# Kernel optimization log

Measured on AMD Instinct MI355X. Metric: run time of the kernel, lower is better.

Reference implementation:

```python
import jax, jax.numpy as jnp
import numpy as np

VOCAB, H, L, NUM_LABELS = 32000, 512, 5, 20


def setup_inputs() -> dict:
    key = jax.random.key(0)
    ks = jax.random.split(key, 8)
    B, T = 64, 512
    inputs = jax.random.randint(ks[0], (B, T), 0, VOCAB, dtype=jnp.int32)
    s = 1.0 / np.sqrt(H)
    emb = jax.random.normal(ks[1], (VOCAB, H), jnp.float32) * 0.02
    emb = emb.at[0].set(0.0)  # padding_idx=0
    W_ih = jax.random.uniform(ks[2], (L, 4 * H, H), jnp.float32, -s, s)
    W_hh = jax.random.uniform(ks[3], (L, 4 * H, H), jnp.float32, -s, s)
    b_ih = jax.random.uniform(ks[4], (L, 4 * H), jnp.float32, -s, s)
    b_hh = jax.random.uniform(ks[5], (L, 4 * H), jnp.float32, -s, s)
    W_cls = jax.random.uniform(ks[6], (NUM_LABELS, H), jnp.float32, -s, s)
    b_cls = jax.random.uniform(ks[7], (NUM_LABELS,), jnp.float32, -s, s)
    return {"inputs": inputs, "emb": emb, "W_ih": W_ih, "W_hh": W_hh,
            "b_ih": b_ih, "b_hh": b_hh, "W_cls": W_cls, "b_cls": b_cls}


def _lstm_layer(x, Wih, Whh, bih, bhh):
    # x: [B, T, H] -> [B, T, H]. PyTorch gate order: i, f, g, o.
    B, T, Hd = x.shape
    xg = jnp.einsum('bth,gh->btg', x, Wih) + bih + bhh  # precompute input gates [B,T,4H]

    def step(carry, xt):
        h, c = carry
        g = xt + h @ Whh.T
        i, f, gg, o = jnp.split(g, 4, axis=-1)
        c = jax.nn.sigmoid(f) * c + jax.nn.sigmoid(i) * jnp.tanh(gg)
        h = jax.nn.sigmoid(o) * jnp.tanh(c)
        return (h, c), h

    h0 = jnp.zeros((B, Hd), x.dtype)
    (_, _), ys = jax.lax.scan(step, (h0, h0), jnp.swapaxes(xg, 0, 1))
    return jnp.swapaxes(ys, 0, 1)


def reference(inputs, emb, W_ih, W_hh, b_ih, b_hh, W_cls, b_cls):
    # Dropout between layers is inactive in eval mode; omitted (deterministic baseline).
    x = emb[inputs]  # [B, T, H]
    for l in range(W_ih.shape[0]):
        x = _lstm_layer(x, W_ih[l], W_hh[l], b_ih[l], b_hh[l])
    feature = x[:, -1]  # last timestep hidden of top layer
    return feature @ W_cls.T + b_cls
```

## Files before the change

kernel.cpp:

```cpp
#include <hip/hip_runtime.h>
#include <cmath>

#define BB 64
#define TT 512
#define HH 512
#define GG 2048
#define TCH 64
#define LDT 132

template<bool GATHER>
__global__ __launch_bounds__(256) void xg_gemm(
    const float* __restrict__ Xsrc, const int* __restrict__ tok,
    const float* __restrict__ Wih, const float* __restrict__ bih,
    const float* __restrict__ bhh, float* __restrict__ XG, int t0)
{
  __shared__ float As[32 * LDT];
  __shared__ float Bs[32 * LDT];
  const int tid = threadIdx.x;
  const int tc = tid & 15, tr = tid >> 4;
  const int m0 = blockIdx.x * 128;
  const int g0 = blockIdx.y * 128;

  float acc[8][8];
#pragma unroll
  for (int i = 0; i < 8; ++i)
#pragma unroll
    for (int j = 0; j < 8; ++j) acc[i][j] = 0.f;

  float4 ra[4], rb[4];
#pragma unroll
  for (int i = 0; i < 4; ++i) {
    const int f = tid + i * 256;
    ra[i] = *(const float4*)&Wih[(size_t)(g0 + (f >> 3)) * HH + ((f & 7) << 2)];
  }
#pragma unroll
  for (int i = 0; i < 4; ++i) {
    const int f = tid + i * 256;
    if (GATHER) {
      const int m = m0 + (f >> 3);
      const int tok_i = tok[(m & 63) * TT + t0 + (m >> 6)];
      rb[i] = *(const float4*)&Xsrc[(size_t)tok_i * HH + ((f & 7) << 2)];
    } else {
      rb[i] = *(const float4*)&Xsrc[((size_t)(t0 + (m0 >> 6) + (f >> 9)) * HH
                                     + ((f >> 4) & 31)) * BB + ((f & 15) << 2)];
    }
  }

  for (int kt = 0; kt < 16; ++kt) {
#pragma unroll
    for (int i = 0; i < 4; ++i) {
      const int f = tid + i * 256;
      const int row = f >> 3, c4 = f & 7, s = c4 & 3;
      const int col = (((row >> 2) ^ s) << 2) + (row & 3);
      As[(c4 * 4 + 0) * LDT + col] = ra[i].x;
      As[(c4 * 4 + 1) * LDT + col] = ra[i].y;
      As[(c4 * 4 + 2) * LDT + col] = ra[i].z;
      As[(c4 * 4 + 3) * LDT + col] = ra[i].w;
    }
#pragma unroll
    for (int i = 0; i < 4; ++i) {
      const int f = tid + i * 256;
      if (GATHER) {
        const int row = f >> 3, c4 = f & 7, s = c4 & 3;
        const int col = (((row >> 2) ^ s) << 2) + (row & 3);
        Bs[(c4 * 4 + 0) * LDT + col] = rb[i].x;
        Bs[(c4 * 4 + 1) * LDT + col] = rb[i].y;
        Bs[(c4 * 4 + 2) * LDT + col] = rb[i].z;
        Bs[(c4 * 4 + 3) * LDT + col] = rb[i].w;
      } else {
        const int kk = (f >> 4) & 31, s = (kk >> 2) & 3;
        const int mq = (((f >> 9) << 4) + (f & 15)) ^ s;
        *(float4*)&Bs[kk * LDT + (mq << 2)] = rb[i];
      }
    }
    __syncthreads();
    if (kt < 15) {
      const int k0 = (kt + 1) * 32;
#pragma unroll
      for (int i = 0; i < 4; ++i) {
        const int f = tid + i * 256;
        ra[i] = *(const float4*)&Wih[(size_t)(g0 + (f >> 3)) * HH + k0 + ((f & 7) << 2)];
      }
#pragma unroll
      for (int i = 0; i < 4; ++i) {
        const int f = tid + i * 256;
        if (GATHER) {
          const int m = m0 + (f >> 3);
          const int tok_i = tok[(m & 63) * TT + t0 + (m >> 6)];
          rb[i] = *(const float4*)&Xsrc[(size_t)tok_i * HH + k0 + ((f & 7) << 2)];
        } else {
          rb[i] = *(const float4*)&Xsrc[((size_t)(t0 + (m0 >> 6) + (f >> 9)) * HH
                                         + k0 + ((f >> 4) & 31)) * BB + ((f & 15) << 2)];
        }
      }
    }
#pragma unroll
    for (int k = 0; k < 32; ++k) {
      const int s = (k >> 2) & 3;
      const float4 a0 = *(const float4*)&As[k * LDT + ((tr ^ s) << 2)];
      const float4 a1 = *(const float4*)&As[k * LDT + ((16 + (tr ^ s)) << 2)];
      const float4 b0 = *(const float4*)&Bs[k * LDT + ((tc ^ s) << 2)];
      const float4 b1 = *(const float4*)&Bs[k * LDT + ((16 + (tc ^ s)) << 2)];
      const float av[8] = {a0.x, a0.y, a0.z, a0.w, a1.x, a1.y, a1.z, a1.w};
      const float bv[8] = {b0.x, b0.y, b0.z, b0.w, b1.x, b1.y, b1.z, b1.w};
#pragma unroll
      for (int i2 = 0; i2 < 8; ++i2)
#pragma unroll
        for (int j2 = 0; j2 < 8; ++j2)
          acc[i2][j2] = fmaf(av[i2], bv[j2], acc[i2][j2]);
    }
    __syncthreads();
  }

#pragma unroll
  for (int ah = 0; ah < 2; ++ah)
#pragma unroll
    for (int i = 0; i < 4; ++i) {
      const int gc = g0 + ah * 64 + tr * 4 + i;
      const float bias = bih[gc] + bhh[gc];
#pragma unroll
      for (int bh = 0; bh < 2; ++bh) {
        const int tl_ = (m0 >> 6) + bh;
        float4 v;
        v.x = acc[ah * 4 + i][bh * 4 + 0] + bias;
        v.y = acc[ah * 4 + i][bh * 4 + 1] + bias;
        v.z = acc[ah * 4 + i][bh * 4 + 2] + bias;
        v.w = acc[ah * 4 + i][bh * 4 + 3] + bias;
        *(float4*)&XG[((size_t)tl_ * GG + gc) * BB + (tc << 2)] = v;
      }
    }
}

__global__ __launch_bounds__(256, 1) void lstm_chunk(
    const float* __restrict__ XG, const float* __restrict__ Whh,
    float* __restrict__ h0, float* __restrict__ h1,
    float* __restrict__ c, float* __restrict__ Y,
    unsigned* __restrict__ bar, int t0, int l)
{
  const int tid = threadIdx.x;
  const int grp = blockIdx.x & 7;
  const int mid = blockIdx.x >> 3;
  const int rp = tid >> 3;
  const int ks = tid & 7;
  const int lr0 = 2 * rp, lr1 = 2 * rp + 1;
  const int gc0 = ((lr0 >> 4) << 9) + mid * 16 + (lr0 & 15);
  const int gc1 = ((lr1 >> 4) << 9) + mid * 16 + (lr1 & 15);

  __shared__ float4 hs4[8 * 136];
  __shared__ float gs[512];

  float4 w0[16], w1[16];
#pragma unroll
  for (int cc = 0; cc < 16; ++cc) {
    w0[cc] = *(const float4*)&Whh[(size_t)gc0 * HH + ks * 64 + cc * 4];
    w1[cc] = *(const float4*)&Whh[(size_t)gc1 * HH + ks * 64 + cc * 4];
  }

  const int hc_l = tid >> 3;
  const int bb_l = tid & 7;
  const int hc_own = mid * 16 + hc_l;
  const int Bg_own = 8 * grp + bb_l;
  float creg = 0.f;
  if (t0 > 0 && tid < 128) creg = c[(size_t)hc_own * BB + Bg_own];

  for (int tl = 0; tl < TCH; ++tl) {
    const int t = t0 + tl;
    const int first = (t == 0) ? 1 : 0;
    const float* h_in = (t & 1) ? h1 : h0;
    float* h_out = (t & 1) ? h0 : h1;

    if (!first) {
#pragma unroll
      for (int i = 0; i < 4; ++i) {
        const int f4 = tid + i * 256;
        const int b = f4 >> 7, c4 = f4 & 127;
        const float* src = &h_in[(size_t)(8 * grp + b) * HH + (c4 << 2)];
        float4 v;
        v.x = __hip_atomic_load(src + 0, __ATOMIC_RELAXED, __HIP_MEMORY_SCOPE_AGENT);
        v.y = __hip_atomic_load(src + 1, __ATOMIC_RELAXED, __HIP_MEMORY_SCOPE_AGENT);
        v.z = __hip_atomic_load(src + 2, __ATOMIC_RELAXED, __HIP_MEMORY_SCOPE_AGENT);
        v.w = __hip_atomic_load(src + 3, __ATOMIC_RELAXED, __HIP_MEMORY_SCOPE_AGENT);
        hs4[b * 136 + c4 + (c4 >> 4)] = v;
      }
      __syncthreads();

      float p0[8], p1[8];
#pragma unroll
      for (int b = 0; b < 8; ++b) { p0[b] = 0.f; p1[b] = 0.f; }
#pragma unroll
      for (int cc = 0; cc < 16; ++cc) {
#pragma unroll
        for (int b = 0; b < 8; ++b) {
          const float4 hv = hs4[b * 136 + 17 * ks + cc];
          p0[b] += hv.x * w0[cc].x + hv.y * w0[cc].y + hv.z * w0[cc].z + hv.w * w0[cc].w;
          p1[b] += hv.x * w1[cc].x + hv.y * w1[cc].y + hv.z * w1[cc].z + hv.w * w1[cc].w;
        }
      }
#pragma unroll
      for (int b = 0; b < 8; ++b) {
        float v0 = p0[b], v1 = p1[b];
        v0 += __shfl_xor(v0, 1, 64); v0 += __shfl_xor(v0, 2, 64); v0 += __shfl_xor(v0, 4, 64);
        v1 += __shfl_xor(v1, 1, 64); v1 += __shfl_xor(v1, 2, 64); v1 += __shfl_xor(v1, 4, 64);
        p0[b] = v0; p1[b] = v1;
      }
      if (ks == 0) {
#pragma unroll
        for (int b = 0; b < 8; ++b) {
          gs[lr0 * 8 + b] = p0[b];
          gs[lr1 * 8 + b] = p1[b];
        }
      }
    }
    __syncthreads();

    if (tid < 128) {
      float gv[4];
#pragma unroll
      for (int q = 0; q < 4; ++q) {
        const int gc = (q << 9) + hc_own;
        float x = XG[((size_t)tl * GG + gc) * BB + Bg_own];
        if (!first) x += gs[(q * 16 + hc_l) * 8 + bb_l];
        gv[q] = x;
      }
      const float cold = first ? 0.f : creg;
      const float si = 1.f / (1.f + expf(-gv[0]));
      const float sf = 1.f / (1.f + expf(-gv[1]));
      const float so = 1.f / (1.f + expf(-gv[3]));
      const float cn = sf * cold + si * tanhf(gv[2]);
      const float hn = so * tanhf(cn);
      creg = cn;
      __hip_atomic_store(&h_out[(size_t)Bg_own * HH + hc_own], hn,
                         __ATOMIC_RELAXED, __HIP_MEMORY_SCOPE_AGENT);
      Y[((size_t)t * HH + hc_own) * BB + Bg_own] = hn;
    }

    asm volatile("s_waitcnt vmcnt(0)" ::: "memory");
    __syncthreads();
    if (tid == 0) {
      __hip_atomic_fetch_add(&bar[grp * 32], 1u, __ATOMIC_RELAXED, __HIP_MEMORY_SCOPE_AGENT);
      const unsigned tgt = 32u * (unsigned)(l * 512 + t + 1);
      while (__hip_atomic_load(&bar[grp * 32], __ATOMIC_RELAXED, __HIP_MEMORY_SCOPE_AGENT) < tgt)
        __builtin_amdgcn_s_sleep(2);
    }
    __syncthreads();
  }

  if (tid < 128) c[(size_t)hc_own * BB + Bg_own] = creg;
}

__global__ __launch_bounds__(64) void cls_kernel(
    const float* __restrict__ Y, const float* __restrict__ Wcls,
    const float* __restrict__ bcls, float* __restrict__ out)
{
  __shared__ float feat[512];
  const int b = blockIdx.x, tid = threadIdx.x;
  for (int k = tid; k < HH; k += 64)
    feat[k] = Y[((size_t)(TT - 1) * HH + k) * BB + b];
  __syncthreads();
  if (tid < 20) {
    float acc = bcls[tid];
    for (int k = 0; k < HH; ++k) acc = fmaf(feat[k], Wcls[tid * HH + k], acc);
    out[b * 20 + tid] = acc;
  }
}

extern "C" void kernel_launch(void* const* d_in, const int* in_sizes, int n_in,
                              void* d_out, int out_size, void* d_ws, size_t ws_size,
                              hipStream_t stream) {
  (void)in_sizes; (void)n_in; (void)out_size; (void)ws_size;
  const int*   tok  = (const int*)d_in[0];
  const float* emb  = (const float*)d_in[1];
  const float* Wih  = (const float*)d_in[2];
  const float* Whh  = (const float*)d_in[3];
  const float* bih  = (const float*)d_in[4];
  const float* bhh  = (const float*)d_in[5];
  const float* Wcls = (const float*)d_in[6];
  const float* bcls = (const float*)d_in[7];
  float* out = (float*)d_out;

  float* Y  = (float*)d_ws;
  float* XG = Y + (size_t)TT * HH * BB;
  float* h0 = XG + (size_t)TCH * GG * BB;
  float* h1 = h0 + (size_t)BB * HH;
  float* c  = h1 + (size_t)BB * HH;
  unsigned* bar = (unsigned*)(c + (size_t)HH * BB);

  hipMemsetAsync(bar, 0, 8 * 32 * sizeof(unsigned), stream);

  for (int l = 0; l < 5; ++l) {
    const float* wih_l = Wih + (size_t)l * GG * HH;
    const float* whh_l = Whh + (size_t)l * GG * HH;
    const float* bih_l = bih + (size_t)l * GG;
    const float* bhh_l = bhh + (size_t)l * GG;
    for (int t0 = 0; t0 < TT; t0 += TCH) {
      if (l == 0)
        xg_gemm<true><<<dim3(32, 16), 256, 0, stream>>>(emb, tok, wih_l, bih_l, bhh_l, XG, t0);
      else
        xg_gemm<false><<<dim3(32, 16), 256, 0, stream>>>(Y, nullptr, wih_l, bih_l, bhh_l, XG, t0);
      lstm_chunk<<<256, 256, 0, stream>>>(XG, whh_l, h0, h1, c, Y, bar, t0, l);
    }
  }
  cls_kernel<<<64, 64, 0, stream>>>(Y, Wcls, bcls, out);
}
```

Baseline: 33.61 ms.

## Replace atomic counter barrier with per-block flags and remap recurrent matvec

Replaces the per-group atomic fetch_add counter barrier with per-block step flags that each block writes and 32 lanes poll in parallel, so arrival no longer serializes on a single contended atomic. The recurrent matvec is remapped: each thread now holds four gate rows over a 32-wide K slice and reduces across 16 lanes, and the hidden-state load uses vectorized dwordx4 loads with cache-bypass bits instead of scalar atomic loads. The XG input gate values are prefetched before the matvec so their latency overlaps with the h load. The risk is higher register pressure from the 4x8 weight tile, extra shuffle reduction steps, and the correctness of the inline-asm coherence bits.

```diff
diff --git a/kernel.cpp b/kernel.cpp
--- a/kernel.cpp
+++ b/kernel.cpp
@@ -135,26 +135,24 @@
     const float* __restrict__ XG, const float* __restrict__ Whh,
     float* __restrict__ h0, float* __restrict__ h1,
     float* __restrict__ c, float* __restrict__ Y,
-    unsigned* __restrict__ bar, int t0, int l)
+    unsigned* __restrict__ flag, int t0, int l)
 {
   const int tid = threadIdx.x;
   const int grp = blockIdx.x & 7;
   const int mid = blockIdx.x >> 3;
-  const int rp = tid >> 3;
-  const int ks = tid & 7;
-  const int lr0 = 2 * rp, lr1 = 2 * rp + 1;
-  const int gc0 = ((lr0 >> 4) << 9) + mid * 16 + (lr0 & 15);
-  const int gc1 = ((lr1 >> 4) << 9) + mid * 16 + (lr1 & 15);
-
-  __shared__ float4 hs4[8 * 136];
+  const int rp = tid >> 4;
+  const int ks = tid & 15;
+
+  __shared__ float4 hs4[8 * 144];
   __shared__ float gs[512];
 
-  float4 w0[16], w1[16];
-#pragma unroll
-  for (int cc = 0; cc < 16; ++cc) {
-    w0[cc] = *(const float4*)&Whh[(size_t)gc0 * HH + ks * 64 + cc * 4];
-    w1[cc] = *(const float4*)&Whh[(size_t)gc1 * HH + ks * 64 + cc * 4];
-  }
+  float4 w[4][8];
+#pragma unroll
+  for (int j = 0; j < 4; ++j)
+#pragma unroll
+    for (int cc = 0; cc < 8; ++cc)
+      w[j][cc] = *(const float4*)&Whh[(size_t)((j << 9) + mid * 16 + rp) * HH
+                                      + ks * 32 + cc * 4];
 
   const int hc_l = tid >> 3;
   const int bb_l = tid & 7;
@@ -169,46 +167,68 @@
     const float* h_in = (t & 1) ? h1 : h0;
     float* h_out = (t & 1) ? h0 : h1;
 
+    float xgv[4];
+    if (tid < 128) {
+#pragma unroll
+      for (int q = 0; q < 4; ++q)
+        xgv[q] = XG[((size_t)tl * GG + (q << 9) + hc_own) * BB + Bg_own];
+    }
+
+    float p[4][8];
+#pragma unroll
+    for (int j = 0; j < 4; ++j)
+#pragma unroll
+      for (int b = 0; b < 8; ++b) p[j][b] = 0.f;
+
     if (!first) {
+      float4 hv4[4];
 #pragma unroll
       for (int i = 0; i < 4; ++i) {
-        const int f4 = tid + i * 256;
-        const int b = f4 >> 7, c4 = f4 & 127;
+        const int f = tid + i * 256;
+        const int b = f >> 7, c4 = f & 127;
         const float* src = &h_in[(size_t)(8 * grp + b) * HH + (c4 << 2)];
-        float4 v;
-        v.x = __hip_atomic_load(src + 0, __ATOMIC_RELAXED, __HIP_MEMORY_SCOPE_AGENT);
-        v.y = __hip_atomic_load(src + 1, __ATOMIC_RELAXED, __HIP_MEMORY_SCOPE_AGENT);
-        v.z = __hip_atomic_load(src + 2, __ATOMIC_RELAXED, __HIP_MEMORY_SCOPE_AGENT);
-        v.w = __hip_atomic_load(src + 3, __ATOMIC_RELAXED, __HIP_MEMORY_SCOPE_AGENT);
-        hs4[b * 136 + c4 + (c4 >> 4)] = v;
+        asm volatile("global_load_dwordx4 %0, %1, off sc0 sc1"
+                     : "=v"(hv4[i]) : "v"(src));
+      }
+      asm volatile("s_waitcnt vmcnt(0)" ::: "memory");
+      __builtin_amdgcn_sched_barrier(0);
+#pragma unroll
+      for (int i = 0; i < 4; ++i) {
+        const int f = tid + i * 256;
+        const int b = f >> 7, c4 = f & 127;
+        hs4[b * 144 + (c4 >> 3) * 9 + (c4 & 7)] = hv4[i];
       }
       __syncthreads();
 
-      float p0[8], p1[8];
-#pragma unroll
-      for (int b = 0; b < 8; ++b) { p0[b] = 0.f; p1[b] = 0.f; }
-#pragma unroll
-      for (int cc = 0; cc < 16; ++cc) {
+#pragma unroll
+      for (int cc = 0; cc < 8; ++cc) {
 #pragma unroll
         for (int b = 0; b < 8; ++b) {
-          const float4 hv = hs4[b * 136 + 17 * ks + cc];
-          p0[b] += hv.x * w0[cc].x + hv.y * w0[cc].y + hv.z * w0[cc].z + hv.w * w0[cc].w;
-          p1[b] += hv.x * w1[cc].x + hv.y * w1[cc].y + hv.z * w1[cc].z + hv.w * w1[cc].w;
+          const float4 hv = hs4[b * 144 + ks * 9 + cc];
+#pragma unroll
+          for (int j = 0; j < 4; ++j) {
+            p[j][b] += hv.x * w[j][cc].x + hv.y * w[j][cc].y
+                     + hv.z * w[j][cc].z + hv.w * w[j][cc].w;
+          }
         }
       }
 #pragma unroll
-      for (int b = 0; b < 8; ++b) {
-        float v0 = p0[b], v1 = p1[b];
-        v0 += __shfl_xor(v0, 1, 64); v0 += __shfl_xor(v0, 2, 64); v0 += __shfl_xor(v0, 4, 64);
-        v1 += __shfl_xor(v1, 1, 64); v1 += __shfl_xor(v1, 2, 64); v1 += __shfl_xor(v1, 4, 64);
-        p0[b] = v0; p1[b] = v1;
-      }
+      for (int j = 0; j < 4; ++j)
+#pragma unroll
+        for (int b = 0; b < 8; ++b) {
+          float v = p[j][b];
+          v += __shfl_xor(v, 1);
+          v += __shfl_xor(v, 2);
+          v += __shfl_xor(v, 4);
+          v += __shfl_xor(v, 8);
+          p[j][b] = v;
+        }
       if (ks == 0) {
 #pragma unroll
-        for (int b = 0; b < 8; ++b) {
-          gs[lr0 * 8 + b] = p0[b];
-          gs[lr1 * 8 + b] = p1[b];
-        }
+        for (int j = 0; j < 4; ++j)
+#pragma unroll
+          for (int b = 0; b < 8; ++b)
+            gs[((j << 4) + rp) * 8 + b] = p[j][b];
       }
     }
     __syncthreads();
@@ -217,8 +237,7 @@
       float gv[4];
 #pragma unroll
       for (int q = 0; q < 4; ++q) {
-        const int gc = (q << 9) + hc_own;
-        float x = XG[((size_t)tl * GG + gc) * BB + Bg_own];
+        float x = xgv[q];
         if (!first) x += gs[(q * 16 + hc_l) * 8 + bb_l];
         gv[q] = x;
       }
@@ -236,11 +255,15 @@
 
     asm volatile("s_waitcnt vmcnt(0)" ::: "memory");
     __syncthreads();
-    if (tid == 0) {
-      __hip_atomic_fetch_add(&bar[grp * 32], 1u, __ATOMIC_RELAXED, __HIP_MEMORY_SCOPE_AGENT);
-      const unsigned tgt = 32u * (unsigned)(l * 512 + t + 1);
-      while (__hip_atomic_load(&bar[grp * 32], __ATOMIC_RELAXED, __HIP_MEMORY_SCOPE_AGENT) < tgt)
-        __builtin_amdgcn_s_sleep(2);
+    const unsigned sid = (unsigned)(l * TT + t + 1);
+    if (tid == 0)
+      __hip_atomic_store(&flag[grp * 32 + mid], sid,
+                         __ATOMIC_RELAXED, __HIP_MEMORY_SCOPE_AGENT);
+    if (tid < 64) {
+      const int fi = grp * 32 + (tid & 31);
+      while (__hip_atomic_load(&flag[fi], __ATOMIC_RELAXED,
+                               __HIP_MEMORY_SCOPE_AGENT) < sid)
+        __builtin_amdgcn_s_sleep(1);
     }
     __syncthreads();
   }
@@ -283,9 +306,9 @@
   float* h0 = XG + (size_t)TCH * GG * BB;
   float* h1 = h0 + (size_t)BB * HH;
   float* c  = h1 + (size_t)BB * HH;
-  unsigned* bar = (unsigned*)(c + (size_t)HH * BB);
-
-  hipMemsetAsync(bar, 0, 8 * 32 * sizeof(unsigned), stream);
+  unsigned* flag = (unsigned*)(c + (size_t)HH * BB);
+
+  hipMemsetAsync(flag, 0, 8 * 32 * sizeof(unsigned), stream);
 
   for (int l = 0; l < 5; ++l) {
     const float* wih_l = Wih + (size_t)l * GG * HH;
@@ -297,7 +320,7 @@
         xg_gemm<true><<<dim3(32, 16), 256, 0, stream>>>(emb, tok, wih_l, bih_l, bhh_l, XG, t0);
       else
         xg_gemm<false><<<dim3(32, 16), 256, 0, stream>>>(Y, nullptr, wih_l, bih_l, bhh_l, XG, t0);
-      lstm_chunk<<<256, 256, 0, stream>>>(XG, whh_l, h0, h1, c, Y, bar, t0, l);
+      lstm_chunk<<<256, 256, 0, stream>>>(XG, whh_l, h0, h1, c, Y, flag, t0, l);
     }
   }
   cls_kernel<<<64, 64, 0, stream>>>(Y, Wcls, bcls, out);
```

Result: slower. 49.18 ms (+46.3%).

## Replace atomic-counter barrier with per-block flags and pipeline h loads

Applied to the files above, without the earlier changes.

Replaces the per-group fetch-add counter barrier with per-block step flags: each block stores its step id to its own slot, and 32 threads poll the 32 flags of the group in parallel. This avoids serialized atomic RMW contention on a single counter per timestep. The h-state loads into LDS are also reordered so two float4 loads stay in flight while earlier values are stored. The polling threads raise read traffic on the flag lines, and the sleep interval is increased.

```diff
diff --git a/kernel.cpp b/kernel.cpp
--- a/kernel.cpp
+++ b/kernel.cpp
@@ -131,11 +131,20 @@
     }
 }
 
+__device__ __forceinline__ float4 ld4a(const float* src) {
+  float4 v;
+  v.x = __hip_atomic_load(src + 0, __ATOMIC_RELAXED, __HIP_MEMORY_SCOPE_AGENT);
+  v.y = __hip_atomic_load(src + 1, __ATOMIC_RELAXED, __HIP_MEMORY_SCOPE_AGENT);
+  v.z = __hip_atomic_load(src + 2, __ATOMIC_RELAXED, __HIP_MEMORY_SCOPE_AGENT);
+  v.w = __hip_atomic_load(src + 3, __ATOMIC_RELAXED, __HIP_MEMORY_SCOPE_AGENT);
+  return v;
+}
+
 __global__ __launch_bounds__(256, 1) void lstm_chunk(
     const float* __restrict__ XG, const float* __restrict__ Whh,
     float* __restrict__ h0, float* __restrict__ h1,
     float* __restrict__ c, float* __restrict__ Y,
-    unsigned* __restrict__ bar, int t0, int l)
+    unsigned* __restrict__ flag, int t0, int l)
 {
   const int tid = threadIdx.x;
   const int grp = blockIdx.x & 7;
@@ -163,6 +172,10 @@
   float creg = 0.f;
   if (t0 > 0 && tid < 128) creg = c[(size_t)hc_own * BB + Bg_own];
 
+  const int sb = tid >> 7;
+  const int sc4 = tid & 127;
+  const int lds_i = sc4 + (sc4 >> 4);
+
   for (int tl = 0; tl < TCH; ++tl) {
     const int t = t0 + tl;
     const int first = (t == 0) ? 1 : 0;
@@ -170,18 +183,18 @@
     float* h_out = (t & 1) ? h0 : h1;
 
     if (!first) {
-#pragma unroll
-      for (int i = 0; i < 4; ++i) {
-        const int f4 = tid + i * 256;
-        const int b = f4 >> 7, c4 = f4 & 127;
-        const float* src = &h_in[(size_t)(8 * grp + b) * HH + (c4 << 2)];
-        float4 v;
-        v.x = __hip_atomic_load(src + 0, __ATOMIC_RELAXED, __HIP_MEMORY_SCOPE_AGENT);
-        v.y = __hip_atomic_load(src + 1, __ATOMIC_RELAXED, __HIP_MEMORY_SCOPE_AGENT);
-        v.z = __hip_atomic_load(src + 2, __ATOMIC_RELAXED, __HIP_MEMORY_SCOPE_AGENT);
-        v.w = __hip_atomic_load(src + 3, __ATOMIC_RELAXED, __HIP_MEMORY_SCOPE_AGENT);
-        hs4[b * 136 + c4 + (c4 >> 4)] = v;
-      }
+      const float* s0 = &h_in[(size_t)(8 * grp + sb + 0) * HH + (sc4 << 2)];
+      const float* s1 = &h_in[(size_t)(8 * grp + sb + 2) * HH + (sc4 << 2)];
+      const float* s2 = &h_in[(size_t)(8 * grp + sb + 4) * HH + (sc4 << 2)];
+      const float* s3 = &h_in[(size_t)(8 * grp + sb + 6) * HH + (sc4 << 2)];
+      float4 va = ld4a(s0);
+      float4 vb = ld4a(s1);
+      hs4[(sb + 0) * 136 + lds_i] = va;
+      va = ld4a(s2);
+      hs4[(sb + 2) * 136 + lds_i] = vb;
+      vb = ld4a(s3);
+      hs4[(sb + 4) * 136 + lds_i] = va;
+      hs4[(sb + 6) * 136 + lds_i] = vb;
       __syncthreads();
 
       float p0[8], p1[8];
@@ -236,11 +249,14 @@
 
     asm volatile("s_waitcnt vmcnt(0)" ::: "memory");
     __syncthreads();
-    if (tid == 0) {
-      __hip_atomic_fetch_add(&bar[grp * 32], 1u, __ATOMIC_RELAXED, __HIP_MEMORY_SCOPE_AGENT);
-      const unsigned tgt = 32u * (unsigned)(l * 512 + t + 1);
-      while (__hip_atomic_load(&bar[grp * 32], __ATOMIC_RELAXED, __HIP_MEMORY_SCOPE_AGENT) < tgt)
-        __builtin_amdgcn_s_sleep(2);
+    const unsigned sid = (unsigned)(l * TT + t + 1);
+    if (tid == 0)
+      __hip_atomic_store(&flag[(grp << 5) + mid], sid,
+                         __ATOMIC_RELAXED, __HIP_MEMORY_SCOPE_AGENT);
+    if (tid < 32) {
+      const unsigned* fp = &flag[(grp << 5) + tid];
+      while (__hip_atomic_load(fp, __ATOMIC_RELAXED, __HIP_MEMORY_SCOPE_AGENT) < sid)
+        __builtin_amdgcn_s_sleep(4);
     }
     __syncthreads();
   }
@@ -283,9 +299,9 @@
   float* h0 = XG + (size_t)TCH * GG * BB;
   float* h1 = h0 + (size_t)BB * HH;
   float* c  = h1 + (size_t)BB * HH;
-  unsigned* bar = (unsigned*)(c + (size_t)HH * BB);
-
-  hipMemsetAsync(bar, 0, 8 * 32 * sizeof(unsigned), stream);
+  unsigned* flag = (unsigned*)(c + (size_t)HH * BB);
+
+  hipMemsetAsync(flag, 0, 256 * sizeof(unsigned), stream);
 
   for (int l = 0; l < 5; ++l) {
     const float* wih_l = Wih + (size_t)l * GG * HH;
@@ -297,7 +313,7 @@
         xg_gemm<true><<<dim3(32, 16), 256, 0, stream>>>(emb, tok, wih_l, bih_l, bhh_l, XG, t0);
       else
         xg_gemm<false><<<dim3(32, 16), 256, 0, stream>>>(Y, nullptr, wih_l, bih_l, bhh_l, XG, t0);
-      lstm_chunk<<<256, 256, 0, stream>>>(XG, whh_l, h0, h1, c, Y, bar, t0, l);
+      lstm_chunk<<<256, 256, 0, stream>>>(XG, whh_l, h0, h1, c, Y, flag, t0, l);
     }
   }
   cls_kernel<<<64, 64, 0, stream>>>(Y, Wcls, bcls, out);
```

Result: no change. 33.02 ms (-1.7%).

## Replace per-step group barrier with step-tagged hidden-state ring polling

Applied to the files above, without the earlier changes.

Each hidden value is now packed with its step id into a 64-bit word in a double-buffered ring. Consumers spin on the data words until every tag matches the expected step, which removes the atomic counter barrier and its extra syncthreads round trip per timestep. The per-step XG input loads are also issued before the wait so their latency overlaps the poll. In exchange, each h load is twice as wide and many threads poll global memory instead of one thread per block.

```diff
diff --git a/kernel.cpp b/kernel.cpp
--- a/kernel.cpp
+++ b/kernel.cpp
@@ -133,9 +133,9 @@
 
 __global__ __launch_bounds__(256, 1) void lstm_chunk(
     const float* __restrict__ XG, const float* __restrict__ Whh,
-    float* __restrict__ h0, float* __restrict__ h1,
+    unsigned long long* __restrict__ ring,
     float* __restrict__ c, float* __restrict__ Y,
-    unsigned* __restrict__ bar, int t0, int l)
+    int t0, int l)
 {
   const int tid = threadIdx.x;
   const int grp = blockIdx.x & 7;
@@ -163,24 +163,51 @@
   float creg = 0.f;
   if (t0 > 0 && tid < 128) creg = c[(size_t)hc_own * BB + Bg_own];
 
+  const int b_st = tid >> 5;
+  const int cq = tid & 31;
+
   for (int tl = 0; tl < TCH; ++tl) {
     const int t = t0 + tl;
     const int first = (t == 0) ? 1 : 0;
-    const float* h_in = (t & 1) ? h1 : h0;
-    float* h_out = (t & 1) ? h0 : h1;
+    const int slot = t & 1;
+
+    float xgv[4];
+    if (tid < 128) {
+#pragma unroll
+      for (int q = 0; q < 4; ++q)
+        xgv[q] = XG[((size_t)tl * GG + (q << 9) + hc_own) * BB + Bg_own];
+    }
 
     if (!first) {
-#pragma unroll
-      for (int i = 0; i < 4; ++i) {
-        const int f4 = tid + i * 256;
-        const int b = f4 >> 7, c4 = f4 & 127;
-        const float* src = &h_in[(size_t)(8 * grp + b) * HH + (c4 << 2)];
+      const unsigned sidp = (unsigned)(l * TT + t);
+      const unsigned long long* src =
+          ring + (size_t)(slot ^ 1) * BB * HH
+               + (size_t)(8 * grp + b_st) * HH + cq * 16;
+      unsigned long long pv[16];
+#pragma unroll
+      for (int j = 0; j < 16; ++j)
+        pv[j] = __hip_atomic_load(&src[j], __ATOMIC_RELAXED, __HIP_MEMORY_SCOPE_AGENT);
+      for (;;) {
+        bool stale = false;
+#pragma unroll
+        for (int j = 0; j < 16; ++j) {
+          if ((unsigned)(pv[j] >> 32) != sidp) {
+            pv[j] = __hip_atomic_load(&src[j], __ATOMIC_RELAXED, __HIP_MEMORY_SCOPE_AGENT);
+            stale = true;
+          }
+        }
+        if (!stale) break;
+        __builtin_amdgcn_s_sleep(1);
+      }
+#pragma unroll
+      for (int q = 0; q < 4; ++q) {
+        const int c4 = cq * 4 + q;
         float4 v;
-        v.x = __hip_atomic_load(src + 0, __ATOMIC_RELAXED, __HIP_MEMORY_SCOPE_AGENT);
-        v.y = __hip_atomic_load(src + 1, __ATOMIC_RELAXED, __HIP_MEMORY_SCOPE_AGENT);
-        v.z = __hip_atomic_load(src + 2, __ATOMIC_RELAXED, __HIP_MEMORY_SCOPE_AGENT);
-        v.w = __hip_atomic_load(src + 3, __ATOMIC_RELAXED, __HIP_MEMORY_SCOPE_AGENT);
-        hs4[b * 136 + c4 + (c4 >> 4)] = v;
+        v.x = __uint_as_float((unsigned)pv[q * 4 + 0]);
+        v.y = __uint_as_float((unsigned)pv[q * 4 + 1]);
+        v.z = __uint_as_float((unsigned)pv[q * 4 + 2]);
+        v.w = __uint_as_float((unsigned)pv[q * 4 + 3]);
+        hs4[b_st * 136 + c4 + (c4 >> 4)] = v;
       }
       __syncthreads();
 
@@ -217,8 +244,7 @@
       float gv[4];
 #pragma unroll
       for (int q = 0; q < 4; ++q) {
-        const int gc = (q << 9) + hc_own;
-        float x = XG[((size_t)tl * GG + gc) * BB + Bg_own];
+        float x = xgv[q];
         if (!first) x += gs[(q * 16 + hc_l) * 8 + bb_l];
         gv[q] = x;
       }
@@ -229,20 +255,13 @@
       const float cn = sf * cold + si * tanhf(gv[2]);
       const float hn = so * tanhf(cn);
       creg = cn;
-      __hip_atomic_store(&h_out[(size_t)Bg_own * HH + hc_own], hn,
-                         __ATOMIC_RELAXED, __HIP_MEMORY_SCOPE_AGENT);
+      const unsigned sid = (unsigned)(l * TT + t + 1);
+      const unsigned long long pk =
+          ((unsigned long long)sid << 32) | (unsigned long long)__float_as_uint(hn);
+      __hip_atomic_store(ring + (size_t)slot * BB * HH + (size_t)Bg_own * HH + hc_own,
+                         pk, __ATOMIC_RELAXED, __HIP_MEMORY_SCOPE_AGENT);
       Y[((size_t)t * HH + hc_own) * BB + Bg_own] = hn;
     }
-
-    asm volatile("s_waitcnt vmcnt(0)" ::: "memory");
-    __syncthreads();
-    if (tid == 0) {
-      __hip_atomic_fetch_add(&bar[grp * 32], 1u, __ATOMIC_RELAXED, __HIP_MEMORY_SCOPE_AGENT);
-      const unsigned tgt = 32u * (unsigned)(l * 512 + t + 1);
-      while (__hip_atomic_load(&bar[grp * 32], __ATOMIC_RELAXED, __HIP_MEMORY_SCOPE_AGENT) < tgt)
-        __builtin_amdgcn_s_sleep(2);
-    }
-    __syncthreads();
   }
 
   if (tid < 128) c[(size_t)hc_own * BB + Bg_own] = creg;
@@ -280,12 +299,10 @@
 
   float* Y  = (float*)d_ws;
   float* XG = Y + (size_t)TT * HH * BB;
-  float* h0 = XG + (size_t)TCH * GG * BB;
-  float* h1 = h0 + (size_t)BB * HH;
-  float* c  = h1 + (size_t)BB * HH;
-  unsigned* bar = (unsigned*)(c + (size_t)HH * BB);
-
-  hipMemsetAsync(bar, 0, 8 * 32 * sizeof(unsigned), stream);
+  float* c  = XG + (size_t)TCH * GG * BB;
+  unsigned long long* ring = (unsigned long long*)(c + (size_t)HH * BB);
+
+  hipMemsetAsync(ring, 0, (size_t)2 * BB * HH * sizeof(unsigned long long), stream);
 
   for (int l = 0; l < 5; ++l) {
     const float* wih_l = Wih + (size_t)l * GG * HH;
@@ -297,7 +314,7 @@
         xg_gemm<true><<<dim3(32, 16), 256, 0, stream>>>(emb, tok, wih_l, bih_l, bhh_l, XG, t0);
       else
         xg_gemm<false><<<dim3(32, 16), 256, 0, stream>>>(Y, nullptr, wih_l, bih_l, bhh_l, XG, t0);
-      lstm_chunk<<<256, 256, 0, stream>>>(XG, whh_l, h0, h1, c, Y, bar, t0, l);
+      lstm_chunk<<<256, 256, 0, stream>>>(XG, whh_l, ring, c, Y, t0, l);
     }
   }
   cls_kernel<<<64, 64, 0, stream>>>(Y, Wcls, bcls, out);
```

New measurement: 56.36 ms. 1.68x slower.
